# Optimization experiments

Measured on AMD Instinct MI355X. Metric: run time of the kernel, lower is better.

The kernel has to match this reference:

```python
import jax, jax.numpy as jnp
import numpy as np

B, S, D = 2, 2048, 1024
H, DH, DL, DR = 16, 64, 512, 64
DHID, N_SHARED, N_ROUTED, TOPK = 512, 2, 8, 2
EPS = 1e-6


def setup_inputs() -> dict:
    key = jax.random.key(0)
    ks = jax.random.split(key, 16)
    w = lambda k, shp: jax.random.normal(k, shp, dtype=jnp.float32) * 0.02
    return {
        "x": jax.random.normal(ks[0], (B, S, D), dtype=jnp.float32),
        "mask": jnp.tril(jnp.ones((S, S), dtype=bool)),  # causal
        "w_q": w(ks[1], (D, H * (DH + DR))),
        "w_dkv": w(ks[2], (D, DL)),
        "w_uk": w(ks[3], (DL, H * DH)),
        "w_uv": w(ks[4], (DL, H * DH)),
        "w_kr": w(ks[5], (D, DR)),
        "w_o": w(ks[6], (H * DH, D)),
        "attn_norm_w": jnp.ones((D,), jnp.float32),
        "mlp_norm_w": jnp.ones((D,), jnp.float32),
        "gate_w": w(ks[7], (D, N_ROUTED)),
        "wr_gate": w(ks[8], (N_ROUTED, D, DHID)),
        "wr_up": w(ks[9], (N_ROUTED, D, DHID)),
        "wr_down": w(ks[10], (N_ROUTED, DHID, D)),
        "ws_gate": w(ks[11], (N_SHARED, D, DHID)),
        "ws_up": w(ks[12], (N_SHARED, D, DHID)),
        "ws_down": w(ks[13], (N_SHARED, DHID, D)),
    }


def _rmsnorm(x, w):
    x32 = x.astype(jnp.float32)
    n = x32 * jax.lax.rsqrt(jnp.mean(x32 * x32, axis=-1, keepdims=True) + EPS)
    return n.astype(x.dtype) * w


def _rope_tables(seq_len, dim):
    half = dim // 2
    inv = 1.0 / (10000.0 ** (jnp.arange(half, dtype=jnp.float32) / half))
    ang = jnp.arange(seq_len, dtype=jnp.float32)[:, None] * inv[None, :]  # [S, dim/2]
    return jnp.cos(ang), jnp.sin(ang)


def _rope(t, cos, sin):
    # t: [..., S, dim]; rotate-half convention
    t1, t2 = jnp.split(t, 2, axis=-1)
    return jnp.concatenate([t1 * cos - t2 * sin, t2 * cos + t1 * sin], axis=-1)


def _layer(x, mask, w_q, w_dkv, w_uk, w_uv, w_kr, w_o, attn_norm_w, mlp_norm_w,
           gate_w, wr_gate, wr_up, wr_down, ws_gate, ws_up, ws_down):
    # ---- pre-norm MLA attention + residual ----
    h = _rmsnorm(x, attn_norm_w)
    cos, sin = _rope_tables(S, DR)

    q = (h @ w_q).reshape(B, S, H, DH + DR).transpose(0, 2, 1, 3)  # [B,H,S,DH+DR]
    q_c, q_r = q[..., :DH], _rope(q[..., DH:], cos, sin)

    latent = h @ w_dkv                                              # [B,S,DL]
    k_c = (latent @ w_uk).reshape(B, S, H, DH).transpose(0, 2, 1, 3)  # [B,H,S,DH]
    v = (latent @ w_uv).reshape(B, S, H, DH).transpose(0, 2, 1, 3)
    k_r = _rope(h @ w_kr, cos, sin)                                 # [B,S,DR] shared across heads

    scale = 1.0 / np.sqrt(DH + DR)
    scores = (jnp.einsum("bhqd,bhkd->bhqk", q_c, k_c)
              + jnp.einsum("bhqd,bkd->bhqk", q_r, k_r)) * scale
    scores = jnp.where(mask, scores, jnp.float32(-1e9))
    attn = jax.nn.softmax(scores, axis=-1)
    ctx = jnp.einsum("bhqk,bhkd->bhqd", attn, v)                    # [B,H,S,DH]
    attn_out = ctx.transpose(0, 2, 1, 3).reshape(B, S, H * DH) @ w_o
    x = x + attn_out

    # ---- pre-norm shared + routed MoE FFN + residual ----
    h = _rmsnorm(x, mlp_norm_w).reshape(-1, D)                      # [T,D]
    probs = jax.nn.softmax(h @ gate_w, axis=-1)                     # [T,NR]
    vals, idx = jax.lax.top_k(probs, TOPK)                          # [T,K]
    gw = vals / jnp.sum(vals, axis=-1, keepdims=True)
    dense_w = jnp.sum(jax.nn.one_hot(idx, N_ROUTED, dtype=h.dtype) * gw[..., None], axis=1)  # [T,NR]

    g = jax.nn.silu(jnp.einsum("td,edh->teh", h, wr_gate))
    u = jnp.einsum("td,edh->teh", h, wr_up)
    y = jnp.einsum("teh,ehd->ted", g * u, wr_down)                  # [T,NR,D]
    routed = jnp.einsum("ted,te->td", y, dense_w)

    gs = jax.nn.silu(jnp.einsum("td,sdh->tsh", h, ws_gate))
    us = jnp.einsum("td,sdh->tsh", h, ws_up)
    shared = jnp.einsum("tsh,shd->td", gs * us, ws_down)

    return x + (routed + shared).reshape(B, S, D)


def reference(x, mask, w_q, w_dkv, w_uk, w_uv, w_kr, w_o, attn_norm_w, mlp_norm_w,
              gate_w, wr_gate, wr_up, wr_down, ws_gate, ws_up, ws_down):
    return _layer(x, mask, w_q, w_dkv, w_uk, w_uv, w_kr, w_o, attn_norm_w, mlp_norm_w,
                  gate_w, wr_gate, wr_up, wr_down, ws_gate, ws_up, ws_down)
```

## Files before the change

kernel.cpp:

```cpp
#include <hip/hip_runtime.h>
#include <hip/hip_bf16.h>
#include <stdint.h>

typedef unsigned short u16;
typedef __attribute__((ext_vector_type(8))) short short8;
typedef __attribute__((ext_vector_type(4))) float f32x4;
typedef __attribute__((ext_vector_type(4))) int i32x4;
typedef __attribute__((ext_vector_type(2))) unsigned int u32x2;

#define B_    2
#define S_    2048
#define D_    1024
#define H_    16
#define T_    (B_*S_)

static __device__ __forceinline__ float b2f(u16 h) { return __uint_as_float(((uint32_t)h) << 16); }
static __device__ __forceinline__ u16 f2b(float f) {
    uint32_t u = __float_as_uint(f);
    u += 0x7fffu + ((u >> 16) & 1u);
    return (u16)(u >> 16);
}
static __device__ __forceinline__ uint32_t pack2(float a, float b) {
    return (uint32_t)f2b(a) | ((uint32_t)f2b(b) << 16);
}
static __device__ __forceinline__ uint32_t cvtpk(float a, float b) {
    uint32_t r;
    asm("v_cvt_pk_bf16_f32 %0, %1, %2" : "=v"(r) : "v"(a), "v"(b));
    return r;
}
#define MFMA(a,b,c) __builtin_amdgcn_mfma_f32_16x16x32_bf16(a,b,c,0,0,0)

static __device__ __forceinline__ void gl2lds16(const void* g, void* l) {
    __builtin_amdgcn_global_load_lds((const __attribute__((address_space(1))) void*)g,
                                     (__attribute__((address_space(3))) void*)l, 16, 0, 0);
}

static __device__ __forceinline__ void tr_body(const float* __restrict__ ip,
    u16* __restrict__ op, int K, int N, int k0, int n0, float (*tile)[33])
{
    int tx = threadIdx.x, ty = threadIdx.y;
#pragma unroll
    for (int i = 0; i < 4; ++i) {
        int k = k0 + ty + 8 * i, n = n0 + tx;
        tile[ty + 8 * i][tx] = (k < K && n < N) ? ip[(long)k * N + n] : 0.f;
    }
    __syncthreads();
#pragma unroll
    for (int i = 0; i < 4; ++i) {
        int n = n0 + ty + 8 * i, k = k0 + tx;
        if (n < N && k < K) op[(long)n * K + k] = f2b(tile[tx][ty + 8 * i]);
    }
}

__global__ __launch_bounds__(256) void transpose_attn_a(const float* __restrict__ wq,
    const float* __restrict__ wdkv, const float* __restrict__ wkr, u16* __restrict__ out)
{
    __shared__ float tile[32][33];
    int bx = blockIdx.x;
    const float* in; u16* op; int N; int n0;
    if (bx < 64)      { in = wq;   op = out;             N = 2048; n0 = bx * 32; }
    else if (bx < 80) { in = wdkv; op = out + 2048*1024; N = 512;  n0 = (bx-64) * 32; }
    else              { in = wkr;  op = out + 2560*1024; N = 64;   n0 = (bx-80) * 32; }
    tr_body(in, op, 1024, N, blockIdx.y * 32, n0, tile);
}

__global__ __launch_bounds__(256) void transpose_attn_b(const float* __restrict__ wuk,
    const float* __restrict__ wuv, const float* __restrict__ wo,
    u16* __restrict__ uk_t, u16* __restrict__ uv_t, u16* __restrict__ wo_t)
{
    __shared__ float tile[32][33];
    int by = blockIdx.y;
    const float* in; u16* op; int K; int k0;
    if (by < 16)      { in = wuk; op = uk_t; K = 512;  k0 = by * 32; }
    else if (by < 32) { in = wuv; op = uv_t; K = 512;  k0 = (by-16) * 32; }
    else              { in = wo;  op = wo_t; K = 1024; k0 = (by-32) * 32; }
    tr_body(in, op, K, 1024, k0, blockIdx.x * 32, tile);
}

__global__ __launch_bounds__(256) void transpose_moe_gu(const float* __restrict__ wr_gate,
    const float* __restrict__ wr_up, const float* __restrict__ ws_gate,
    const float* __restrict__ ws_up, u16* __restrict__ wgu_t)
{
    __shared__ float tile[32][33];
    int z = blockIdx.z;
    const float* in; u16* op;
    if (z < 8)       { in = wr_gate + (long)z * 524288;      op = wgu_t + (long)z * 1048576; }
    else if (z < 16) { in = wr_up   + (long)(z-8) * 524288;  op = wgu_t + (long)(z-8) * 1048576 + 524288; }
    else if (z < 18) { in = ws_gate + (long)(z-16) * 524288; op = wgu_t + (long)(z-8) * 1048576; }
    else             { in = ws_up   + (long)(z-18) * 524288; op = wgu_t + (long)(z-10) * 1048576 + 524288; }
    tr_body(in, op, 1024, 512, blockIdx.y * 32, blockIdx.x * 32, tile);
}

__global__ __launch_bounds__(256) void transpose_moe_down(const float* __restrict__ wr_down,
    const float* __restrict__ ws_down, u16* __restrict__ wd_t)
{
    __shared__ float tile[32][33];
    int z = blockIdx.z;
    const float* in = (z < 8) ? wr_down + (long)z * 524288 : ws_down + (long)(z-8) * 524288;
    u16* op = wd_t + (long)z * 524288;
    tr_body(in, op, 512, 1024, blockIdx.y * 32, blockIdx.x * 32, tile);
}

__global__ __launch_bounds__(256) void gemm_k(const u16* __restrict__ A, long lda,
    const u16* __restrict__ Bt, long ldb, void* __restrict__ Cv, long ldc, int K,
    int mode, const float* __restrict__ resid)
{
    __shared__ u16 As[3][128 * 32];
    __shared__ u16 Bs[3][128 * 32];
    const int tid = threadIdx.x, lane = tid & 63, wave = tid >> 6;
    const int wm = (wave & 1) * 64, wn = (wave >> 1) * 64;
    const int quad = lane >> 4, rr = lane & 15, q8 = quad * 8;
    const long row0 = (long)blockIdx.y * 128, col0 = (long)blockIdx.x * 128;
    f32x4 acc[4][4];
#pragma unroll
    for (int i = 0; i < 4; ++i)
#pragma unroll
        for (int j = 0; j < 4; ++j)
#pragma unroll
            for (int c = 0; c < 4; ++c) acc[i][j][c] = 0.f;
    const int band = wave * 32;
    const u16* ga = A + (row0 + band + (lane >> 2)) * lda + (lane & 3) * 8;
    const u16* gb = Bt + (col0 + band + (lane >> 2)) * ldb + (lane & 3) * 8;
    const int lo = band * 32;
    const int nt = K >> 5;
#define STG(bi, k0s) do { \
    gl2lds16(ga + (k0s), &As[bi][lo]); \
    gl2lds16(ga + (k0s) + 16 * lda, &As[bi][lo + 512]); \
    gl2lds16(gb + (k0s), &Bs[bi][lo]); \
    gl2lds16(gb + (k0s) + 16 * ldb, &Bs[bi][lo + 512]); } while (0)
    STG(0, 0);
    STG(1, 32);
    asm volatile("s_waitcnt vmcnt(4)" ::: "memory");
    __builtin_amdgcn_s_barrier();
    int cur = 0, nx2 = 2;
    for (int t = 0; t < nt; ++t) {
        const bool more = (t + 2 < nt);
        if (more) STG(nx2, (t + 2) * 32);
        short8 af[4], bf[4];
#pragma unroll
        for (int mi = 0; mi < 4; ++mi) af[mi] = *(const short8*)&As[cur][(wm + mi * 16 + rr) * 32 + q8];
#pragma unroll
        for (int ni = 0; ni < 4; ++ni) bf[ni] = *(const short8*)&Bs[cur][(wn + ni * 16 + rr) * 32 + q8];
#pragma unroll
        for (int mi = 0; mi < 4; ++mi)
#pragma unroll
            for (int ni = 0; ni < 4; ++ni)
                acc[mi][ni] = MFMA(af[mi], bf[ni], acc[mi][ni]);
        if (more) asm volatile("s_waitcnt vmcnt(4)" ::: "memory");
        else      asm volatile("s_waitcnt vmcnt(0)" ::: "memory");
        __builtin_amdgcn_s_barrier();
        cur = (cur == 2) ? 0 : cur + 1;
        nx2 = (nx2 == 2) ? 0 : nx2 + 1;
    }
#undef STG
#pragma unroll
    for (int mi = 0; mi < 4; ++mi)
#pragma unroll
        for (int ni = 0; ni < 4; ++ni)
#pragma unroll
            for (int rg = 0; rg < 4; ++rg) {
                long r = row0 + wm + mi * 16 + quad * 4 + rg;
                long c = col0 + wn + ni * 16 + rr;
                float v = acc[mi][ni][rg];
                if (mode == 1)      ((u16*)Cv)[r * ldc + c] = f2b(v);
                else if (mode == 2) ((float*)Cv)[r * ldc + c] += v;
                else                ((float*)Cv)[r * ldc + c] = v + resid[r * 1024 + c];
            }
}

__global__ __launch_bounds__(256) void gemm_dual(
    const u16* __restrict__ A0, long lda0, const u16* __restrict__ B0, long ldb0, u16* __restrict__ C0, long ldc0, int nx0, int ny0,
    const u16* __restrict__ A1, long lda1, const u16* __restrict__ B1, long ldb1, u16* __restrict__ C1, long ldc1, int nx1, int ny1)
{
    const int z = blockIdx.z;
    if ((int)blockIdx.x >= (z ? nx1 : nx0) || (int)blockIdx.y >= (z ? ny1 : ny0)) return;
    const u16* A  = z ? A1 : A0;  const long lda = z ? lda1 : lda0;
    const u16* Bt = z ? B1 : B0;  const long ldb = z ? ldb1 : ldb0;
    u16* C = z ? C1 : C0;         const long ldc = z ? ldc1 : ldc0;
    __shared__ u16 As[3][128 * 32];
    __shared__ u16 Bs[3][128 * 32];
    const int tid = threadIdx.x, lane = tid & 63, wave = tid >> 6;
    const int wm = (wave & 1) * 64, wn = (wave >> 1) * 64;
    const int quad = lane >> 4, rr = lane & 15, q8 = quad * 8;
    const long row0 = (long)blockIdx.y * 128, col0 = (long)blockIdx.x * 128;
    f32x4 acc[4][4];
#pragma unroll
    for (int i = 0; i < 4; ++i)
#pragma unroll
        for (int j = 0; j < 4; ++j)
#pragma unroll
            for (int c = 0; c < 4; ++c) acc[i][j][c] = 0.f;
    const int band = wave * 32;
    const u16* ga = A + (row0 + band + (lane >> 2)) * lda + (lane & 3) * 8;
    const u16* gb = Bt + (col0 + band + (lane >> 2)) * ldb + (lane & 3) * 8;
    const int lo = band * 32;
    const int nt = 16;
#define STG(bi, k0s) do { \
    gl2lds16(ga + (k0s), &As[bi][lo]); \
    gl2lds16(ga + (k0s) + 16 * lda, &As[bi][lo + 512]); \
    gl2lds16(gb + (k0s), &Bs[bi][lo]); \
    gl2lds16(gb + (k0s) + 16 * ldb, &Bs[bi][lo + 512]); } while (0)
    STG(0, 0);
    STG(1, 32);
    asm volatile("s_waitcnt vmcnt(4)" ::: "memory");
    __builtin_amdgcn_s_barrier();
    int cur = 0, nx2 = 2;
    for (int t = 0; t < nt; ++t) {
        const bool more = (t + 2 < nt);
        if (more) STG(nx2, (t + 2) * 32);
        short8 af[4], bf[4];
#pragma unroll
        for (int mi = 0; mi < 4; ++mi) af[mi] = *(const short8*)&As[cur][(wm + mi * 16 + rr) * 32 + q8];
#pragma unroll
        for (int ni = 0; ni < 4; ++ni) bf[ni] = *(const short8*)&Bs[cur][(wn + ni * 16 + rr) * 32 + q8];
#pragma unroll
        for (int mi = 0; mi < 4; ++mi)
#pragma unroll
            for (int ni = 0; ni < 4; ++ni)
                acc[mi][ni] = MFMA(af[mi], bf[ni], acc[mi][ni]);
        if (more) asm volatile("s_waitcnt vmcnt(4)" ::: "memory");
        else      asm volatile("s_waitcnt vmcnt(0)" ::: "memory");
        __builtin_amdgcn_s_barrier();
        cur = (cur == 2) ? 0 : cur + 1;
        nx2 = (nx2 == 2) ? 0 : nx2 + 1;
    }
#undef STG
#pragma unroll
    for (int mi = 0; mi < 4; ++mi)
#pragma unroll
        for (int ni = 0; ni < 4; ++ni)
#pragma unroll
            for (int rg = 0; rg < 4; ++rg) {
                long r = row0 + wm + mi * 16 + quad * 4 + rg;
                long c = col0 + wn + ni * 16 + rr;
                C[r * ldc + c] = f2b(acc[mi][ni][rg]);
            }
}

__global__ __launch_bounds__(256) void gemm_guall(const u16* __restrict__ H2,
    const u16* __restrict__ BtAll, u16* __restrict__ gu_r, u16* __restrict__ gu_s,
    const int* __restrict__ cnt, const int* __restrict__ off, const int* __restrict__ elist)
{
    const int e = blockIdx.z;
    const bool sh = (e >= 8);
    const int cntE = sh ? 4096 : cnt[e];
    const int offE = sh ? 0 : off[e];
    const int m0 = blockIdx.y * 128;
    if (m0 >= cntE) return;
    const u16* Bt = BtAll + (long)e * 1048576;
    __shared__ u16 As[3][128 * 32];
    __shared__ u16 Bs[3][128 * 32];
    const int tid = threadIdx.x, lane = tid & 63, wave = tid >> 6;
    const int wm = (wave & 1) * 64, wn = (wave >> 1) * 64;
    const int quad = lane >> 4, rr = lane & 15, q8 = quad * 8;
    const long col0 = (long)blockIdx.x * 128;
    f32x4 acc[4][4];
#pragma unroll
    for (int i = 0; i < 4; ++i)
#pragma unroll
        for (int j = 0; j < 4; ++j)
#pragma unroll
            for (int c = 0; c < 4; ++c) acc[i][j][c] = 0.f;
    const int band = wave * 32;
    int r0 = m0 + band + (lane >> 2);
    int r1 = r0 + 16;
    int tok0, tok1;
    if (sh) { tok0 = r0; tok1 = r1; }
    else {
        tok0 = elist[offE + (r0 < cntE ? r0 : cntE - 1)];
        tok1 = elist[offE + (r1 < cntE ? r1 : cntE - 1)];
    }
    const u16* ga0 = H2 + (long)tok0 * 1024 + (lane & 3) * 8;
    const u16* ga1 = H2 + (long)tok1 * 1024 + (lane & 3) * 8;
    const u16* gb = Bt + (col0 + band + (lane >> 2)) * 1024L + (lane & 3) * 8;
    const int lo = band * 32;
#define STG(bi, k0s) do { \
    gl2lds16(ga0 + (k0s), &As[bi][lo]); \
    gl2lds16(ga1 + (k0s), &As[bi][lo + 512]); \
    gl2lds16(gb + (k0s), &Bs[bi][lo]); \
    gl2lds16(gb + (k0s) + 16 * 1024, &Bs[bi][lo + 512]); } while (0)
    const int nt = 32;
    STG(0, 0);
    STG(1, 32);
    asm volatile("s_waitcnt vmcnt(4)" ::: "memory");
    __builtin_amdgcn_s_barrier();
    int cur = 0, nx2 = 2;
    for (int t = 0; t < nt; ++t) {
        const bool more = (t + 2 < nt);
        if (more) STG(nx2, (t + 2) * 32);
        short8 af[4], bf[4];
#pragma unroll
        for (int mi = 0; mi < 4; ++mi) af[mi] = *(const short8*)&As[cur][(wm + mi * 16 + rr) * 32 + q8];
#pragma unroll
        for (int ni = 0; ni < 4; ++ni) bf[ni] = *(const short8*)&Bs[cur][(wn + ni * 16 + rr) * 32 + q8];
#pragma unroll
        for (int mi = 0; mi < 4; ++mi)
#pragma unroll
            for (int ni = 0; ni < 4; ++ni)
                acc[mi][ni] = MFMA(af[mi], bf[ni], acc[mi][ni]);
        if (more) asm volatile("s_waitcnt vmcnt(4)" ::: "memory");
        else      asm volatile("s_waitcnt vmcnt(0)" ::: "memory");
        __builtin_amdgcn_s_barrier();
        cur = (cur == 2) ? 0 : cur + 1;
        nx2 = (nx2 == 2) ? 0 : nx2 + 1;
    }
#undef STG
#pragma unroll
    for (int mi = 0; mi < 4; ++mi)
#pragma unroll
        for (int ni = 0; ni < 4; ++ni)
#pragma unroll
            for (int rg = 0; rg < 4; ++rg) {
                int ml = wm + mi * 16 + quad * 4 + rg;
                long c = col0 + wn + ni * 16 + rr;
                if (m0 + ml < cntE) {
                    float v = acc[mi][ni][rg];
                    if (sh) gu_s[(long)(m0 + ml) * 2048 + (long)(e - 8) * 1024 + c] = f2b(v);
                    else    gu_r[(long)(offE + m0 + ml) * 1024 + c] = f2b(v);
                }
            }
}

__global__ __launch_bounds__(256) void gemm_downall(const u16* __restrict__ gu_r,
    const u16* __restrict__ gu_s, const u16* __restrict__ WdAll, u16* __restrict__ rout,
    float* __restrict__ xmid, const int* __restrict__ cnt, const int* __restrict__ off)
{
    const int e = blockIdx.z;
    __shared__ u16 As[3][128 * 32];
    __shared__ u16 Bs[3][128 * 32];
    const int tid = threadIdx.x, lane = tid & 63, wave = tid >> 6;
    const int wm = (wave & 1) * 64, wn = (wave >> 1) * 64;
    const int quad = lane >> 4, rr = lane & 15, q8 = quad * 8;
    const long col0 = (long)blockIdx.x * 128;
    const int m0 = blockIdx.y * 128;
    const int band = wave * 32;
    const int lo = band * 32;
    f32x4 acc[4][4];
#pragma unroll
    for (int i = 0; i < 4; ++i)
#pragma unroll
        for (int j = 0; j < 4; ++j)
#pragma unroll
            for (int c = 0; c < 4; ++c) acc[i][j][c] = 0.f;
    if (e < 8) {
        const int cntE = cnt[e], offE = off[e];
        if (m0 >= cntE) return;
        const u16* Bt = WdAll + (long)e * 524288;
        int r0 = offE + m0 + band + (lane >> 2); if (r0 > 8191) r0 = 8191;
        int r1 = r0 + 16; if (r1 > 8191) r1 = 8191;
        const u16* ga0 = gu_r + (long)r0 * 1024 + (lane & 3) * 8;
        const u16* ga1 = gu_r + (long)r1 * 1024 + (lane & 3) * 8;
        const u16* gb = Bt + (col0 + band + (lane >> 2)) * 512L + (lane & 3) * 8;
#define STGR(bi, k0s) do { \
    gl2lds16(ga0 + (k0s), &As[bi][lo]); \
    gl2lds16(ga1 + (k0s), &As[bi][lo + 512]); \
    gl2lds16(gb + (k0s), &Bs[bi][lo]); \
    gl2lds16(gb + (k0s) + 16 * 512, &Bs[bi][lo + 512]); } while (0)
        const int nt = 16;
        STGR(0, 0);
        STGR(1, 32);
        asm volatile("s_waitcnt vmcnt(4)" ::: "memory");
        __builtin_amdgcn_s_barrier();
        int cur = 0, nx2 = 2;
        for (int t = 0; t < nt; ++t) {
            const bool more = (t + 2 < nt);
            if (more) STGR(nx2, (t + 2) * 32);
            short8 af[4], bf[4];
#pragma unroll
            for (int mi = 0; mi < 4; ++mi) af[mi] = *(const short8*)&As[cur][(wm + mi * 16 + rr) * 32 + q8];
#pragma unroll
            for (int ni = 0; ni < 4; ++ni) bf[ni] = *(const short8*)&Bs[cur][(wn + ni * 16 + rr) * 32 + q8];
#pragma unroll
            for (int mi = 0; mi < 4; ++mi)
#pragma unroll
                for (int ni = 0; ni < 4; ++ni)
                    acc[mi][ni] = MFMA(af[mi], bf[ni], acc[mi][ni]);
            if (more) asm volatile("s_waitcnt vmcnt(4)" ::: "memory");
            else      asm volatile("s_waitcnt vmcnt(0)" ::: "memory");
            __builtin_amdgcn_s_barrier();
            cur = (cur == 2) ? 0 : cur + 1;
            nx2 = (nx2 == 2) ? 0 : nx2 + 1;
        }
#undef STGR
#pragma unroll
        for (int mi = 0; mi < 4; ++mi)
#pragma unroll
            for (int ni = 0; ni < 4; ++ni)
#pragma unroll
                for (int rg = 0; rg < 4; ++rg) {
                    int ml = wm + mi * 16 + quad * 4 + rg;
                    long c = col0 + wn + ni * 16 + rr;
                    if (m0 + ml < cntE)
                        rout[(long)(offE + m0 + ml) * 1024 + c] = f2b(acc[mi][ni][rg]);
                }
    } else {
        const u16* BtBase = WdAll + 8L * 524288;
        const long arow = m0 + band + (lane >> 2);
        const long brow = col0 + band + (lane >> 2);
#define STGS(bi, k0s) do { \
    const long aoff = ((k0s) < 512) ? (long)(k0s) : (long)(512 + (k0s)); \
    const long boff = ((k0s) < 512) ? (long)(k0s) : (long)(524288 - 512 + (k0s)); \
    const u16* ga = gu_s + arow * 2048 + aoff + (lane & 3) * 8; \
    const u16* gb = BtBase + brow * 512 + boff + (lane & 3) * 8; \
    gl2lds16(ga, &As[bi][lo]); \
    gl2lds16(ga + 16 * 2048, &As[bi][lo + 512]); \
    gl2lds16(gb, &Bs[bi][lo]); \
    gl2lds16(gb + 16 * 512, &Bs[bi][lo + 512]); } while (0)
        const int nt = 32;
        STGS(0, 0);
        STGS(1, 32);
        asm volatile("s_waitcnt vmcnt(4)" ::: "memory");
        __builtin_amdgcn_s_barrier();
        int cur = 0, nx2 = 2;
        for (int t = 0; t < nt; ++t) {
            const bool more = (t + 2 < nt);
            if (more) STGS(nx2, (t + 2) * 32);
            short8 af[4], bf[4];
#pragma unroll
            for (int mi = 0; mi < 4; ++mi) af[mi] = *(const short8*)&As[cur][(wm + mi * 16 + rr) * 32 + q8];
#pragma unroll
            for (int ni = 0; ni < 4; ++ni) bf[ni] = *(const short8*)&Bs[cur][(wn + ni * 16 + rr) * 32 + q8];
#pragma unroll
            for (int mi = 0; mi < 4; ++mi)
#pragma unroll
                for (int ni = 0; ni < 4; ++ni)
                    acc[mi][ni] = MFMA(af[mi], bf[ni], acc[mi][ni]);
            if (more) asm volatile("s_waitcnt vmcnt(4)" ::: "memory");
            else      asm volatile("s_waitcnt vmcnt(0)" ::: "memory");
            __builtin_amdgcn_s_barrier();
            cur = (cur == 2) ? 0 : cur + 1;
            nx2 = (nx2 == 2) ? 0 : nx2 + 1;
        }
#undef STGS
#pragma unroll
        for (int mi = 0; mi < 4; ++mi)
#pragma unroll
            for (int ni = 0; ni < 4; ++ni)
#pragma unroll
                for (int rg = 0; rg < 4; ++rg) {
                    long r = m0 + wm + mi * 16 + quad * 4 + rg;
                    long c = col0 + wn + ni * 16 + rr;
                    xmid[r * 1024 + c] += acc[mi][ni][rg];
                }
    }
}

__global__ __launch_bounds__(256) void rmsnorm_wave(const float* __restrict__ x,
    const float* __restrict__ w, u16* __restrict__ out)
{
    const int t = blockIdx.x * 4 + (threadIdx.x >> 6);
    const int lane = threadIdx.x & 63;
    const float* xp = x + (size_t)t * D_;
    f32x4 v[4];
    float s = 0.f;
#pragma unroll
    for (int i = 0; i < 4; ++i) {
        v[i] = *(const f32x4*)&xp[lane * 4 + i * 256];
#pragma unroll
        for (int j = 0; j < 4; ++j) s += v[i][j] * v[i][j];
    }
#pragma unroll
    for (int o = 32; o > 0; o >>= 1) s += __shfl_xor(s, o);
    const float inv = rsqrtf(s * (1.f / D_) + 1e-6f);
    u16* op = out + (size_t)t * D_;
#pragma unroll
    for (int i = 0; i < 4; ++i) {
        const int d = lane * 4 + i * 256;
        f32x4 wv = *(const f32x4*)&w[d];
        u32x2 pk;
        pk[0] = pack2(v[i][0] * inv * wv[0], v[i][1] * inv * wv[1]);
        pk[1] = pack2(v[i][2] * inv * wv[2], v[i][3] * inv * wv[3]);
        *(u32x2*)&op[d] = pk;
    }
}

__global__ __launch_bounds__(256) void rmsnorm_gate_fused(const float* __restrict__ xm,
    const float* __restrict__ nw, const float* __restrict__ gw, u16* __restrict__ h2,
    int* __restrict__ tok_e, float* __restrict__ tok_w)
{
    const int t = blockIdx.x * 4 + (threadIdx.x >> 6);
    const int lane = threadIdx.x & 63;
    const float* xp = xm + (size_t)t * D_;
    f32x4 v[4];
    float s = 0.f;
#pragma unroll
    for (int i = 0; i < 4; ++i) {
        v[i] = *(const f32x4*)&xp[lane * 4 + i * 256];
#pragma unroll
        for (int j = 0; j < 4; ++j) s += v[i][j] * v[i][j];
    }
#pragma unroll
    for (int o = 32; o > 0; o >>= 1) s += __shfl_xor(s, o);
    const float inv = rsqrtf(s * (1.f / D_) + 1e-6f);
    u16* op = h2 + (size_t)t * D_;
    float part[8] = {0,0,0,0,0,0,0,0};
#pragma unroll
    for (int i = 0; i < 4; ++i) {
        const int d = lane * 4 + i * 256;
        f32x4 wv = *(const f32x4*)&nw[d];
        float hv[4];
#pragma unroll
        for (int j = 0; j < 4; ++j) hv[j] = v[i][j] * inv * wv[j];
        u32x2 pk;
        pk[0] = pack2(hv[0], hv[1]);
        pk[1] = pack2(hv[2], hv[3]);
        *(u32x2*)&op[d] = pk;
#pragma unroll
        for (int j = 0; j < 4; ++j) {
            const float* gp = gw + (size_t)(d + j) * 8;
#pragma unroll
            for (int e = 0; e < 8; ++e) part[e] += hv[j] * gp[e];
        }
    }
#pragma unroll
    for (int e = 0; e < 8; ++e)
#pragma unroll
        for (int o = 32; o > 0; o >>= 1) part[e] += __shfl_xor(part[e], o);
    if (lane == 0) {
        float mx = part[0];
#pragma unroll
        for (int e = 1; e < 8; ++e) mx = fmaxf(mx, part[e]);
        float p[8];
#pragma unroll
        for (int e = 0; e < 8; ++e) p[e] = __expf(part[e] - mx);
        int i0 = 0;
#pragma unroll
        for (int e = 1; e < 8; ++e) if (p[e] > p[i0]) i0 = e;
        int i1 = (i0 == 0) ? 1 : 0;
#pragma unroll
        for (int e = 0; e < 8; ++e) { if (e == i0) continue; if (p[e] > p[i1]) i1 = e; }
        float sw = p[i0] + p[i1];
        tok_e[2 * t] = i0;  tok_e[2 * t + 1] = i1;
        tok_w[2 * t] = p[i0] / sw;  tok_w[2 * t + 1] = p[i1] / sw;
    }
}

__global__ __launch_bounds__(256) void moe_route(const int* __restrict__ tok_e,
    int* __restrict__ cnt, int* __restrict__ off,
    int* __restrict__ elist, int* __restrict__ tslot)
{
    const int E = blockIdx.x;
    const int tid = threadIdx.x, lane = tid & 63, wave = tid >> 6;
    int ev[32];
#pragma unroll
    for (int i = 0; i < 8; ++i)
        *(i32x4*)&ev[i * 4] = *(const i32x4*)&tok_e[tid * 32 + i * 4];
    int c8[8] = {0,0,0,0,0,0,0,0};
#pragma unroll
    for (int k = 0; k < 32; ++k) ++c8[ev[k] & 7];
    int incl[8];
#pragma unroll
    for (int e = 0; e < 8; ++e) {
        int vv = c8[e];
#pragma unroll
        for (int d = 1; d < 64; d <<= 1) {
            int tmp = __shfl_up(vv, d);
            if (lane >= d) vv += tmp;
        }
        incl[e] = vv;
    }
    __shared__ int wtot[4][8];
    if (lane == 63)
#pragma unroll
        for (int e = 0; e < 8; ++e) wtot[wave][e] = incl[e];
    __syncthreads();
    int tot[8];
#pragma unroll
    for (int e = 0; e < 8; ++e) tot[e] = wtot[0][e] + wtot[1][e] + wtot[2][e] + wtot[3][e];
    int waveoff = 0;
    for (int w = 0; w < 4; ++w) if (w < wave) waveoff += wtot[w][E];
    int offE = 0;
#pragma unroll
    for (int e = 0; e < 8; ++e) if (e < E) offE += tot[e];
    int rank = offE + waveoff + (incl[E] - c8[E]);
#pragma unroll
    for (int k = 0; k < 32; ++k) {
        if ((ev[k] & 7) == E) {
            int p = tid * 32 + k;
            elist[rank] = p >> 1;
            tslot[p] = rank;
            ++rank;
        }
    }
    if (tid == 0) { cnt[E] = tot[E]; off[E] = offE; }
}

__global__ __launch_bounds__(256) void rope_all(u16* __restrict__ proj)
{
    int idx = blockIdx.x * 256 + threadIdx.x;
    int i = idx & 31;
    int r = idx >> 5;
    int t = r / 17, which = r - t * 17;
    int s = t & (S_ - 1);
    float inv = __expf(-(float)i * 0.28782313662425575f);
    float ang = (float)s * inv;
    float c = cosf(ang), sn = sinf(ang);
    u16* base = proj + (size_t)t * 2688 + (which < 16 ? which * 128 + 64 : 2560);
    float t1 = b2f(base[i]), t2 = b2f(base[32 + i]);
    base[i]      = f2b(t1 * c - t2 * sn);
    base[32 + i] = f2b(t2 * c + t1 * sn);
}

__global__ __launch_bounds__(256, 4) void attn_flash(const u16* __restrict__ proj,
    const u16* __restrict__ kc, const u16* __restrict__ vt, u16* __restrict__ ctx)
{
    const int qidx = blockIdx.x >> 5;
    const int qt = (qidx < 8) ? (31 - qidx) : (qidx < 16) ? (qidx - 8)
                 : (qidx < 24) ? (39 - qidx) : (qidx - 16);
    const int bh = blockIdx.x & 31;
    const int b = bh >> 4, h = bh & 15;
    const int q0 = qt * 64;
    const int tid = threadIdx.x, lane = tid & 63, wave = tid >> 6;
    const int quad = lane >> 4, rr = lane & 15, q8 = quad * 8;
    const int wm2 = wave * 16;

    __shared__ u16 Ks[64 * 128];
    __shared__ u16 Ps[64 * 64];

    const long tbase = (long)b * S_ + q0;
    short8 qf[4];
#pragma unroll
    for (int d0 = 0; d0 < 4; ++d0)
        qf[d0] = *(const short8*)&proj[(tbase + wm2 + rr) * 2688 + h * 128 + d0 * 32 + q8];

    f32x4 accO[4];
    float m_i = -3e38f, l_i = 0.f;
#pragma unroll
    for (int vi = 0; vi < 4; ++vi)
#pragma unroll
        for (int rg = 0; rg < 4; ++rg) accO[vi][rg] = 0.f;
    const float sc = 0.08838834764831845f * 1.4426950408889634f;

    const int srow0 = tid >> 3, sg = tid & 7;
    const int swz = sg ^ (srow0 & 7);
    const u16* kcp = kc   + ((long)b * S_ + srow0) * 1024 + h * 64 + sg * 8;
    const u16* krp = proj + ((long)b * S_ + srow0) * 2688 + 2560 + sg * 8;
    const u16* vbase = vt + (size_t)(h * 64 + rr) * 4096 + b * 2048 + q8;
    const int rg7 = rr & 7;
    int rdcol[4];
#pragma unroll
    for (int d0 = 0; d0 < 4; ++d0) rdcol[d0] = ((d0 * 4 + quad) ^ rg7) * 8;
    const int prcol0 = (((quad * 16) ^ (rg7 << 4)) >> 1);
    const int prcol1 = (((64 + quad * 16) ^ (rg7 << 4)) >> 1);

    const int nkt = qt + 1;
    short8 rk0 = *(const short8*)(kcp);
    short8 rk1 = *(const short8*)(kcp + 32 * 1024);
    short8 rm0 = *(const short8*)(krp);
    short8 rm1 = *(const short8*)(krp + (size_t)32 * 2688);

    for (int kt = 0; kt < nkt; ++kt) {
        const int k0 = kt * 64;
        *(short8*)&Ks[srow0 * 128 + swz * 8]             = rk0;
        *(short8*)&Ks[(srow0 + 32) * 128 + swz * 8]      = rk1;
        *(short8*)&Ks[srow0 * 128 + 64 + swz * 8]        = rm0;
        *(short8*)&Ks[(srow0 + 32) * 128 + 64 + swz * 8] = rm1;
        __syncthreads();

        const size_t k0s = (kt + 1 < nkt) ? (size_t)(k0 + 64) : 0;
        short8 nk0 = *(const short8*)(kcp + k0s * 1024);
        short8 nk1 = *(const short8*)(kcp + k0s * 1024 + 32 * 1024);
        short8 nm0 = *(const short8*)(krp + k0s * 2688);
        short8 nm1 = *(const short8*)(krp + k0s * 2688 + (size_t)32 * 2688);

        f32x4 accS[4];
#pragma unroll
        for (int ki = 0; ki < 4; ++ki)
#pragma unroll
            for (int rg = 0; rg < 4; ++rg) accS[ki][rg] = 0.f;
        __builtin_amdgcn_s_setprio(1);
#pragma unroll
        for (int d0 = 0; d0 < 4; ++d0) {
            short8 kf[4];
#pragma unroll
            for (int ki = 0; ki < 4; ++ki) kf[ki] = *(const short8*)&Ks[(ki * 16 + rr) * 128 + rdcol[d0]];
#pragma unroll
            for (int ki = 0; ki < 4; ++ki) accS[ki] = MFMA(kf[ki], qf[d0], accS[ki]);
        }
        __builtin_amdgcn_s_setprio(0);
        __syncthreads();

        short8 vf0[4], vf1[4];
#pragma unroll
        for (int vi = 0; vi < 4; ++vi) {
            vf0[vi] = *(const short8*)(vbase + (size_t)vi * 16 * 4096 + k0);
            vf1[vi] = *(const short8*)(vbase + (size_t)vi * 16 * 4096 + k0 + 32);
        }

        float mx = -3e38f;
        if (kt == qt) {
            const int qg = q0 + wm2 + rr;
#pragma unroll
            for (int ki = 0; ki < 4; ++ki)
#pragma unroll
                for (int rg = 0; rg < 4; ++rg) {
                    float w = accS[ki][rg] * sc;
                    if (k0 + ki * 16 + quad * 4 + rg > qg) w = -1e30f;
                    accS[ki][rg] = w;
                    mx = fmaxf(mx, w);
                }
        } else {
#pragma unroll
            for (int ki = 0; ki < 4; ++ki)
#pragma unroll
                for (int rg = 0; rg < 4; ++rg) {
                    float w = accS[ki][rg] * sc;
                    accS[ki][rg] = w;
                    mx = fmaxf(mx, w);
                }
        }
        mx = fmaxf(mx, __shfl_xor(mx, 16));
        mx = fmaxf(mx, __shfl_xor(mx, 32));
        if (__any(mx > m_i)) {
            float mnew = fmaxf(m_i, mx);
            float alpha = exp2f(m_i - mnew);
            m_i = mnew;
            l_i *= alpha;
#pragma unroll
            for (int vi = 0; vi < 4; ++vi)
#pragma unroll
                for (int rg = 0; rg < 4; ++rg) accO[vi][rg] *= alpha;
        }
        float ps = 0.f;
#pragma unroll
        for (int ki = 0; ki < 4; ++ki) {
            float p0 = exp2f(accS[ki][0] - m_i);
            float p1 = exp2f(accS[ki][1] - m_i);
            float p2 = exp2f(accS[ki][2] - m_i);
            float p3 = exp2f(accS[ki][3] - m_i);
            ps += (p0 + p1) + (p2 + p3);
            u32x2 pk; pk[0] = cvtpk(p0, p1); pk[1] = cvtpk(p2, p3);
            *(u32x2*)&Ps[(wm2 + rr) * 64 + ((((ki * 32 + quad * 8) ^ (rg7 << 4)) >> 1))] = pk;
        }
        ps += __shfl_xor(ps, 16);
        ps += __shfl_xor(ps, 32);
        l_i += ps;

        short8 pf0 = *(const short8*)&Ps[(wm2 + rr) * 64 + prcol0];
        short8 pf1 = *(const short8*)&Ps[(wm2 + rr) * 64 + prcol1];
        __builtin_amdgcn_s_setprio(1);
#pragma unroll
        for (int vi = 0; vi < 4; ++vi) accO[vi] = MFMA(vf0[vi], pf0, accO[vi]);
#pragma unroll
        for (int vi = 0; vi < 4; ++vi) accO[vi] = MFMA(vf1[vi], pf1, accO[vi]);
        __builtin_amdgcn_s_setprio(0);

        rk0 = nk0; rk1 = nk1; rm0 = nm0; rm1 = nm1;
    }
    {
        float linv = 1.f / l_i;
        long t = tbase + wm2 + rr;
#pragma unroll
        for (int vi = 0; vi < 4; ++vi) {
            u32x2 pk;
            pk[0] = pack2(accO[vi][0] * linv, accO[vi][1] * linv);
            pk[1] = pack2(accO[vi][2] * linv, accO[vi][3] * linv);
            *(u32x2*)&ctx[t * 1024 + h * 64 + vi * 16 + quad * 4] = pk;
        }
    }
}

__global__ __launch_bounds__(256) void silu_all(u16* __restrict__ gu_r, u16* __restrict__ gu_s)
{
    int i = blockIdx.x * 256 + threadIdx.x;
    int row = i >> 6, j8 = (i & 63) * 8;
    u16* gu = (row < 8192) ? gu_r + (long)row * 1024 : gu_s + (long)(row - 8192) * 1024;
    short8 g8 = *(const short8*)&gu[j8];
    short8 u8 = *(const short8*)&gu[512 + j8];
    short8 r;
#pragma unroll
    for (int j = 0; j < 8; ++j) {
        float g = b2f((u16)g8[j]), u = b2f((u16)u8[j]);
        r[j] = (short)f2b(g / (1.f + __expf(-g)) * u);
    }
    *(short8*)&gu[j8] = r;
}

__global__ __launch_bounds__(256) void final_kernel(const float* __restrict__ xm,
    const u16* __restrict__ rout, const int* __restrict__ tok_slot,
    const float* __restrict__ tok_w, float* __restrict__ out)
{
    long i = ((long)blockIdx.x * 256 + threadIdx.x) * 4;
    int t = (int)(i >> 10), d = (int)(i & 1023);
    int s0 = tok_slot[2 * t], s1 = tok_slot[2 * t + 1];
    float w0 = tok_w[2 * t], w1 = tok_w[2 * t + 1];
    f32x4 xv = *(const f32x4*)&xm[i];
    u32x2 r0 = *(const u32x2*)&rout[(long)s0 * 1024 + d];
    u32x2 r1 = *(const u32x2*)&rout[(long)s1 * 1024 + d];
    f32x4 o;
    o[0] = xv[0] + w0 * b2f((u16)(r0[0] & 0xffffu)) + w1 * b2f((u16)(r1[0] & 0xffffu));
    o[1] = xv[1] + w0 * b2f((u16)(r0[0] >> 16))     + w1 * b2f((u16)(r1[0] >> 16));
    o[2] = xv[2] + w0 * b2f((u16)(r0[1] & 0xffffu)) + w1 * b2f((u16)(r1[1] & 0xffffu));
    o[3] = xv[3] + w0 * b2f((u16)(r0[1] >> 16))     + w1 * b2f((u16)(r1[1] >> 16));
    *(f32x4*)&out[i] = o;
}

#define OFF_XMID   0UL
#define OFF_H      16777216UL
#define OFF_PROJ   25165824UL
#define OFF_WGU    25165824UL
#define OFF_KC     47185920UL
#define OFF_WD     47185920UL
#define OFF_VT     55574528UL
#define OFF_GUR    57671680UL
#define OFF_CTX    63963136UL
#define OFF_WATT   72351744UL
#define OFF_ROUT   74448896UL
#define OFF_GUS    91226112UL
#define OFF_TOKE   108003328UL
#define OFF_TOKW   108036096UL
#define OFF_TSLOT  108068864UL
#define OFF_ELIST  108101632UL
#define OFF_META   108134400UL

extern "C" void kernel_launch(void* const* d_in, const int* in_sizes, int n_in,
                              void* d_out, int out_size, void* d_ws, size_t ws_size,
                              hipStream_t stream)
{
    const float* x       = (const float*)d_in[0];
    const float* w_q     = (const float*)d_in[2];
    const float* w_dkv   = (const float*)d_in[3];
    const float* w_uk    = (const float*)d_in[4];
    const float* w_uv    = (const float*)d_in[5];
    const float* w_kr    = (const float*)d_in[6];
    const float* w_o     = (const float*)d_in[7];
    const float* attn_nw = (const float*)d_in[8];
    const float* mlp_nw  = (const float*)d_in[9];
    const float* gate_w  = (const float*)d_in[10];
    const float* wr_gate = (const float*)d_in[11];
    const float* wr_up   = (const float*)d_in[12];
    const float* wr_down = (const float*)d_in[13];
    const float* ws_gate = (const float*)d_in[14];
    const float* ws_up   = (const float*)d_in[15];
    const float* ws_down = (const float*)d_in[16];
    float* out = (float*)d_out;

    char* W = (char*)d_ws;
    float* x_mid = (float*)(W + OFF_XMID);
    u16* h      = (u16*)(W + OFF_H);
    u16* h2     = (u16*)(W + OFF_H);
    u16* proj   = (u16*)(W + OFF_PROJ);
    u16* wgu_t  = (u16*)(W + OFF_WGU);
    u16* kc     = (u16*)(W + OFF_KC);
    u16* wd_t   = (u16*)(W + OFF_WD);
    u16* vt     = (u16*)(W + OFF_VT);
    u16* gu_r   = (u16*)(W + OFF_GUR);
    u16* ctx    = (u16*)(W + OFF_CTX);
    u16* wqkv_t = (u16*)(W + OFF_WATT);
    u16* wuk_t  = wqkv_t + 2688 * 1024;
    u16* wuv_t  = wuk_t + 1024 * 512;
    u16* wo_t   = wuv_t + 1024 * 512;
    u16* rout   = (u16*)(W + OFF_ROUT);
    u16* gu_s   = (u16*)(W + OFF_GUS);
    int*   tok_e = (int*)(W + OFF_TOKE);
    float* tok_w = (float*)(W + OFF_TOKW);
    int*   tslot = (int*)(W + OFF_TSLOT);
    int*   elist = (int*)(W + OFF_ELIST);
    int*   meta  = (int*)(W + OFF_META);
    int* cnt = meta, * off = meta + 8;

    dim3 tb(32, 8);
    transpose_attn_a<<<dim3(82, 32), tb, 0, stream>>>(w_q, w_dkv, w_kr, wqkv_t);
    transpose_attn_b<<<dim3(32, 64), tb, 0, stream>>>(w_uk, w_uv, w_o, wuk_t, wuv_t, wo_t);

    rmsnorm_wave<<<T_ / 4, 256, 0, stream>>>(x, attn_nw, h);
    gemm_k<<<dim3(21, 32), 256, 0, stream>>>(h, 1024, wqkv_t, 1024, proj, 2688, 1024, 1, nullptr);
    rope_all<<<(T_ * 17 * 32) / 256, 256, 0, stream>>>(proj);
    gemm_dual<<<dim3(32, 32, 2), 256, 0, stream>>>(
        proj + 2048, 2688, wuk_t, 512, kc, 1024, 8, 32,
        wuv_t, 512, proj + 2048, 2688, vt, 4096, 32, 8);
    attn_flash<<<1024, 256, 0, stream>>>(proj, kc, vt, ctx);
    gemm_k<<<dim3(8, 32), 256, 0, stream>>>(ctx, 1024, wo_t, 1024, x_mid, 1024, 1024, 3, x);

    transpose_moe_gu<<<dim3(16, 32, 20), tb, 0, stream>>>(wr_gate, wr_up, ws_gate, ws_up, wgu_t);
    transpose_moe_down<<<dim3(32, 16, 10), tb, 0, stream>>>(wr_down, ws_down, wd_t);

    rmsnorm_gate_fused<<<T_ / 4, 256, 0, stream>>>(x_mid, mlp_nw, gate_w, h2, tok_e, tok_w);
    moe_route<<<8, 256, 0, stream>>>(tok_e, cnt, off, elist, tslot);
    gemm_guall<<<dim3(8, 32, 10), 256, 0, stream>>>(h2, wgu_t, gu_r, gu_s, cnt, off, elist);
    silu_all<<<(16384 * 64) / 256, 256, 0, stream>>>(gu_r, gu_s);
    gemm_downall<<<dim3(8, 32, 9), 256, 0, stream>>>(gu_r, gu_s, wd_t, rout, x_mid, cnt, off);
    final_kernel<<<(T_ * D_) / 1024, 256, 0, stream>>>(x_mid, rout, tslot, tok_w, out);
}
```

Before: 525.4 us.

## Fuse RoPE into QKV GEMM epilogue and SwiGLU into gate/up GEMM

```diff
diff --git a/kernel.cpp b/kernel.cpp
--- a/kernel.cpp
+++ b/kernel.cpp
@@ -49,6 +49,24 @@
     for (int i = 0; i < 4; ++i) {
         int n = n0 + ty + 8 * i, k = k0 + tx;
         if (n < N && k < K) op[(long)n * K + k] = f2b(tile[tx][ty + 8 * i]);
+    }
+}
+
+static __device__ __forceinline__ void tr_body_perm(const float* __restrict__ ip,
+    u16* __restrict__ op, int k0, int n0, int is_up, float (*tile)[33])
+{
+    int tx = threadIdx.x, ty = threadIdx.y;
+#pragma unroll
+    for (int i = 0; i < 4; ++i) {
+        int k = k0 + ty + 8 * i, n = n0 + tx;
+        tile[ty + 8 * i][tx] = ip[(long)k * 512 + n];
+    }
+    __syncthreads();
+#pragma unroll
+    for (int i = 0; i < 4; ++i) {
+        int n = n0 + ty + 8 * i, k = k0 + tx;
+        int nr = 128 * (n >> 6) + 64 * ((n >> 5) & 1) + (is_up ? 32 : 0) + (n & 31);
+        op[(long)nr * 1024 + k] = f2b(tile[tx][ty + 8 * i]);
     }
 }
 
@@ -77,33 +95,33 @@
     tr_body(in, op, K, 1024, k0, blockIdx.x * 32, tile);
 }
 
-__global__ __launch_bounds__(256) void transpose_moe_gu(const float* __restrict__ wr_gate,
+__global__ __launch_bounds__(256) void transpose_moe(const float* __restrict__ wr_gate,
     const float* __restrict__ wr_up, const float* __restrict__ ws_gate,
-    const float* __restrict__ ws_up, u16* __restrict__ wgu_t)
+    const float* __restrict__ ws_up, const float* __restrict__ wr_down,
+    const float* __restrict__ ws_down, u16* __restrict__ wgu_t, u16* __restrict__ wd_t)
 {
     __shared__ float tile[32][33];
     int z = blockIdx.z;
-    const float* in; u16* op;
-    if (z < 8)       { in = wr_gate + (long)z * 524288;      op = wgu_t + (long)z * 1048576; }
-    else if (z < 16) { in = wr_up   + (long)(z-8) * 524288;  op = wgu_t + (long)(z-8) * 1048576 + 524288; }
-    else if (z < 18) { in = ws_gate + (long)(z-16) * 524288; op = wgu_t + (long)(z-8) * 1048576; }
-    else             { in = ws_up   + (long)(z-18) * 524288; op = wgu_t + (long)(z-10) * 1048576 + 524288; }
-    tr_body(in, op, 1024, 512, blockIdx.y * 32, blockIdx.x * 32, tile);
-}
-
-__global__ __launch_bounds__(256) void transpose_moe_down(const float* __restrict__ wr_down,
-    const float* __restrict__ ws_down, u16* __restrict__ wd_t)
-{
-    __shared__ float tile[32][33];
-    int z = blockIdx.z;
-    const float* in = (z < 8) ? wr_down + (long)z * 524288 : ws_down + (long)(z-8) * 524288;
-    u16* op = wd_t + (long)z * 524288;
-    tr_body(in, op, 512, 1024, blockIdx.y * 32, blockIdx.x * 32, tile);
+    if (z < 20) {
+        if (blockIdx.x >= 16) return;
+        const float* in; u16* op; int is_up;
+        if (z < 8)       { in = wr_gate + (long)z * 524288;      op = wgu_t + (long)z * 1048576;      is_up = 0; }
+        else if (z < 16) { in = wr_up   + (long)(z-8) * 524288;  op = wgu_t + (long)(z-8) * 1048576;  is_up = 1; }
+        else if (z < 18) { in = ws_gate + (long)(z-16) * 524288; op = wgu_t + (long)(z-8) * 1048576;  is_up = 0; }
+        else             { in = ws_up   + (long)(z-18) * 524288; op = wgu_t + (long)(z-10) * 1048576; is_up = 1; }
+        tr_body_perm(in, op, blockIdx.y * 32, blockIdx.x * 32, is_up, tile);
+    } else {
+        if (blockIdx.y >= 16) return;
+        int zz = z - 20;
+        const float* in = (zz < 8) ? wr_down + (long)zz * 524288 : ws_down + (long)(zz-8) * 524288;
+        u16* op = wd_t + (long)zz * 524288;
+        tr_body(in, op, 512, 1024, blockIdx.y * 32, blockIdx.x * 32, tile);
+    }
 }
 
 __global__ __launch_bounds__(256) void gemm_k(const u16* __restrict__ A, long lda,
     const u16* __restrict__ Bt, long ldb, void* __restrict__ Cv, long ldc, int K,
-    int mode, const float* __restrict__ resid)
+    int mode, const float* __restrict__ resid, int ropeflg)
 {
     __shared__ u16 As[3][128 * 32];
     __shared__ u16 Bs[3][128 * 32];
@@ -153,6 +171,24 @@
         nx2 = (nx2 == 2) ? 0 : nx2 + 1;
     }
 #undef STG
+    if (ropeflg && (((int)blockIdx.x < 16 && wn == 64) || ((int)blockIdx.x == 20 && wn == 0))) {
+#pragma unroll
+        for (int ni = 0; ni < 2; ++ni) {
+            const int i = ni * 16 + rr;
+            const float inv = __expf(-(float)i * 0.28782313662425575f);
+#pragma unroll
+            for (int mi = 0; mi < 4; ++mi)
+#pragma unroll
+                for (int rg = 0; rg < 4; ++rg) {
+                    int srow = (int)((row0 + wm + mi * 16 + quad * 4 + rg) & (S_ - 1));
+                    float ang = (float)srow * inv;
+                    float cc = cosf(ang), ss = sinf(ang);
+                    float t1 = acc[mi][ni][rg], t2 = acc[mi][ni + 2][rg];
+                    acc[mi][ni][rg]     = t1 * cc - t2 * ss;
+                    acc[mi][ni + 2][rg] = t2 * cc + t1 * ss;
+                }
+        }
+    }
 #pragma unroll
     for (int mi = 0; mi < 4; ++mi)
 #pragma unroll
@@ -238,7 +274,7 @@
 }
 
 __global__ __launch_bounds__(256) void gemm_guall(const u16* __restrict__ H2,
-    const u16* __restrict__ BtAll, u16* __restrict__ gu_r, u16* __restrict__ gu_s,
+    const u16* __restrict__ BtAll, u16* __restrict__ act_r, u16* __restrict__ act_s,
     const int* __restrict__ cnt, const int* __restrict__ off, const int* __restrict__ elist)
 {
     const int e = blockIdx.z;
@@ -253,7 +289,6 @@
     const int tid = threadIdx.x, lane = tid & 63, wave = tid >> 6;
     const int wm = (wave & 1) * 64, wn = (wave >> 1) * 64;
     const int quad = lane >> 4, rr = lane & 15, q8 = quad * 8;
-    const long col0 = (long)blockIdx.x * 128;
     f32x4 acc[4][4];
 #pragma unroll
     for (int i = 0; i < 4; ++i)
@@ -272,7 +307,7 @@
     }
     const u16* ga0 = H2 + (long)tok0 * 1024 + (lane & 3) * 8;
     const u16* ga1 = H2 + (long)tok1 * 1024 + (lane & 3) * 8;
-    const u16* gb = Bt + (col0 + band + (lane >> 2)) * 1024L + (lane & 3) * 8;
+    const u16* gb = Bt + ((long)blockIdx.x * 128 + band + (lane >> 2)) * 1024L + (lane & 3) * 8;
     const int lo = band * 32;
 #define STG(bi, k0s) do { \
     gl2lds16(ga0 + (k0s), &As[bi][lo]); \
@@ -308,21 +343,21 @@
 #pragma unroll
     for (int mi = 0; mi < 4; ++mi)
 #pragma unroll
-        for (int ni = 0; ni < 4; ++ni)
+        for (int ni = 0; ni < 2; ++ni)
 #pragma unroll
             for (int rg = 0; rg < 4; ++rg) {
                 int ml = wm + mi * 16 + quad * 4 + rg;
-                long c = col0 + wn + ni * 16 + rr;
-                if (m0 + ml < cntE) {
-                    float v = acc[mi][ni][rg];
-                    if (sh) gu_s[(long)(m0 + ml) * 2048 + (long)(e - 8) * 1024 + c] = f2b(v);
-                    else    gu_r[(long)(offE + m0 + ml) * 1024 + c] = f2b(v);
-                }
+                if (m0 + ml >= cntE) continue;
+                int cout = 64 * (int)blockIdx.x + 32 * (wn >> 6) + ni * 16 + rr;
+                float g = acc[mi][ni][rg], u = acc[mi][ni + 2][rg];
+                float val = g / (1.f + __expf(-g)) * u;
+                if (sh) act_s[(long)(m0 + ml) * 1024 + (long)(e - 8) * 512 + cout] = f2b(val);
+                else    act_r[(long)(offE + m0 + ml) * 512 + cout] = f2b(val);
             }
 }
 
-__global__ __launch_bounds__(256) void gemm_downall(const u16* __restrict__ gu_r,
-    const u16* __restrict__ gu_s, const u16* __restrict__ WdAll, u16* __restrict__ rout,
+__global__ __launch_bounds__(256) void gemm_downall(const u16* __restrict__ act_r,
+    const u16* __restrict__ act_s, const u16* __restrict__ WdAll, u16* __restrict__ rout,
     float* __restrict__ xmid, const int* __restrict__ cnt, const int* __restrict__ off)
 {
     const int e = blockIdx.z;
@@ -348,8 +383,8 @@
         const u16* Bt = WdAll + (long)e * 524288;
         int r0 = offE + m0 + band + (lane >> 2); if (r0 > 8191) r0 = 8191;
         int r1 = r0 + 16; if (r1 > 8191) r1 = 8191;
-        const u16* ga0 = gu_r + (long)r0 * 1024 + (lane & 3) * 8;
-        const u16* ga1 = gu_r + (long)r1 * 1024 + (lane & 3) * 8;
+        const u16* ga0 = act_r + (long)r0 * 512 + (lane & 3) * 8;
+        const u16* ga1 = act_r + (long)r1 * 512 + (lane & 3) * 8;
         const u16* gb = Bt + (col0 + band + (lane >> 2)) * 512L + (lane & 3) * 8;
 #define STGR(bi, k0s) do { \
     gl2lds16(ga0 + (k0s), &As[bi][lo]); \
@@ -398,12 +433,11 @@
         const long arow = m0 + band + (lane >> 2);
         const long brow = col0 + band + (lane >> 2);
 #define STGS(bi, k0s) do { \
-    const long aoff = ((k0s) < 512) ? (long)(k0s) : (long)(512 + (k0s)); \
     const long boff = ((k0s) < 512) ? (long)(k0s) : (long)(524288 - 512 + (k0s)); \
-    const u16* ga = gu_s + arow * 2048 + aoff + (lane & 3) * 8; \
+    const u16* ga = act_s + arow * 1024 + (k0s) + (lane & 3) * 8; \
     const u16* gb = BtBase + brow * 512 + boff + (lane & 3) * 8; \
     gl2lds16(ga, &As[bi][lo]); \
-    gl2lds16(ga + 16 * 2048, &As[bi][lo + 512]); \
+    gl2lds16(ga + 16 * 1024, &As[bi][lo + 512]); \
     gl2lds16(gb, &Bs[bi][lo]); \
     gl2lds16(gb + 16 * 512, &Bs[bi][lo + 512]); } while (0)
         const int nt = 32;
@@ -585,22 +619,6 @@
     if (tid == 0) { cnt[E] = tot[E]; off[E] = offE; }
 }
 
-__global__ __launch_bounds__(256) void rope_all(u16* __restrict__ proj)
-{
-    int idx = blockIdx.x * 256 + threadIdx.x;
-    int i = idx & 31;
-    int r = idx >> 5;
-    int t = r / 17, which = r - t * 17;
-    int s = t & (S_ - 1);
-    float inv = __expf(-(float)i * 0.28782313662425575f);
-    float ang = (float)s * inv;
-    float c = cosf(ang), sn = sinf(ang);
-    u16* base = proj + (size_t)t * 2688 + (which < 16 ? which * 128 + 64 : 2560);
-    float t1 = b2f(base[i]), t2 = b2f(base[32 + i]);
-    base[i]      = f2b(t1 * c - t2 * sn);
-    base[32 + i] = f2b(t2 * c + t1 * sn);
-}
-
 __global__ __launch_bounds__(256, 4) void attn_flash(const u16* __restrict__ proj,
     const u16* __restrict__ kc, const u16* __restrict__ vt, u16* __restrict__ ctx)
 {
@@ -758,22 +776,6 @@
             *(u32x2*)&ctx[t * 1024 + h * 64 + vi * 16 + quad * 4] = pk;
         }
     }
-}
-
-__global__ __launch_bounds__(256) void silu_all(u16* __restrict__ gu_r, u16* __restrict__ gu_s)
-{
-    int i = blockIdx.x * 256 + threadIdx.x;
-    int row = i >> 6, j8 = (i & 63) * 8;
-    u16* gu = (row < 8192) ? gu_r + (long)row * 1024 : gu_s + (long)(row - 8192) * 1024;
-    short8 g8 = *(const short8*)&gu[j8];
-    short8 u8 = *(const short8*)&gu[512 + j8];
-    short8 r;
-#pragma unroll
-    for (int j = 0; j < 8; ++j) {
-        float g = b2f((u16)g8[j]), u = b2f((u16)u8[j]);
-        r[j] = (short)f2b(g / (1.f + __expf(-g)) * u);
-    }
-    *(short8*)&gu[j8] = r;
 }
 
 __global__ __launch_bounds__(256) void final_kernel(const float* __restrict__ xm,
@@ -844,14 +846,14 @@
     u16* kc     = (u16*)(W + OFF_KC);
     u16* wd_t   = (u16*)(W + OFF_WD);
     u16* vt     = (u16*)(W + OFF_VT);
-    u16* gu_r   = (u16*)(W + OFF_GUR);
+    u16* act_r  = (u16*)(W + OFF_GUR);
     u16* ctx    = (u16*)(W + OFF_CTX);
     u16* wqkv_t = (u16*)(W + OFF_WATT);
     u16* wuk_t  = wqkv_t + 2688 * 1024;
     u16* wuv_t  = wuk_t + 1024 * 512;
     u16* wo_t   = wuv_t + 1024 * 512;
     u16* rout   = (u16*)(W + OFF_ROUT);
-    u16* gu_s   = (u16*)(W + OFF_GUS);
+    u16* act_s  = (u16*)(W + OFF_GUS);
     int*   tok_e = (int*)(W + OFF_TOKE);
     float* tok_w = (float*)(W + OFF_TOKW);
     int*   tslot = (int*)(W + OFF_TSLOT);
@@ -864,21 +866,19 @@
     transpose_attn_b<<<dim3(32, 64), tb, 0, stream>>>(w_uk, w_uv, w_o, wuk_t, wuv_t, wo_t);
 
     rmsnorm_wave<<<T_ / 4, 256, 0, stream>>>(x, attn_nw, h);
-    gemm_k<<<dim3(21, 32), 256, 0, stream>>>(h, 1024, wqkv_t, 1024, proj, 2688, 1024, 1, nullptr);
-    rope_all<<<(T_ * 17 * 32) / 256, 256, 0, stream>>>(proj);
+    gemm_k<<<dim3(21, 32), 256, 0, stream>>>(h, 1024, wqkv_t, 1024, proj, 2688, 1024, 1, nullptr, 1);
     gemm_dual<<<dim3(32, 32, 2), 256, 0, stream>>>(
         proj + 2048, 2688, wuk_t, 512, kc, 1024, 8, 32,
         wuv_t, 512, proj + 2048, 2688, vt, 4096, 32, 8);
     attn_flash<<<1024, 256, 0, stream>>>(proj, kc, vt, ctx);
-    gemm_k<<<dim3(8, 32), 256, 0, stream>>>(ctx, 1024, wo_t, 1024, x_mid, 1024, 1024, 3, x);
-
-    transpose_moe_gu<<<dim3(16, 32, 20), tb, 0, stream>>>(wr_gate, wr_up, ws_gate, ws_up, wgu_t);
-    transpose_moe_down<<<dim3(32, 16, 10), tb, 0, stream>>>(wr_down, ws_down, wd_t);
+    gemm_k<<<dim3(8, 32), 256, 0, stream>>>(ctx, 1024, wo_t, 1024, x_mid, 1024, 1024, 3, x, 0);
+
+    transpose_moe<<<dim3(32, 32, 30), tb, 0, stream>>>(wr_gate, wr_up, ws_gate, ws_up,
+                                                       wr_down, ws_down, wgu_t, wd_t);
 
     rmsnorm_gate_fused<<<T_ / 4, 256, 0, stream>>>(x_mid, mlp_nw, gate_w, h2, tok_e, tok_w);
     moe_route<<<8, 256, 0, stream>>>(tok_e, cnt, off, elist, tslot);
-    gemm_guall<<<dim3(8, 32, 10), 256, 0, stream>>>(h2, wgu_t, gu_r, gu_s, cnt, off, elist);
-    silu_all<<<(16384 * 64) / 256, 256, 0, stream>>>(gu_r, gu_s);
-    gemm_downall<<<dim3(8, 32, 9), 256, 0, stream>>>(gu_r, gu_s, wd_t, rout, x_mid, cnt, off);
+    gemm_guall<<<dim3(8, 32, 10), 256, 0, stream>>>(h2, wgu_t, act_r, act_s, cnt, off, elist);
+    gemm_downall<<<dim3(8, 32, 9), 256, 0, stream>>>(act_r, act_s, wd_t, rout, x_mid, cnt, off);
     final_kernel<<<(T_ * D_) / 1024, 256, 0, stream>>>(x_mid, rout, tslot, tok_w, out);
 }
```

Result: slower. 551.5 us (+5.0%).
